# Optimization experiments

Measured on AMD Instinct MI355X. Metric: run time of the kernel, lower is better.

## Reference

```python
import jax, jax.numpy as jnp
import numpy as np

B, D, H, W_ = 2, 256, 64, 64


def setup_inputs() -> dict:
    key = jax.random.key(0)
    k1, k2 = jax.random.split(key)
    x = jax.random.normal(k1, (B, D, H, W_), dtype=jnp.float32)
    W = jax.random.normal(k2, (3 * D, D), dtype=jnp.float32) * 0.02  # 1x1 conv weight [out,in]
    b = jnp.zeros((3 * D,), dtype=jnp.float32)
    return {"x": x, "W": W, "b": b}


def reference(x, W, b):
    Bs, d, h, w = x.shape
    N = h * w
    sqrtV = d ** 0.25  # sqrt(sqrt(d)); q,k each divided -> qk^T / sqrt(d)
    # 1x1 conv == per-pixel linear over channels
    qkv = jnp.einsum('bchw,oc->bohw', x, W) + b[None, :, None, None]
    q, k, v = jnp.split(qkv, 3, axis=1)
    q = q.reshape(Bs, d, N).transpose(0, 2, 1) / sqrtV  # [B,N,d]
    k = k.reshape(Bs, d, N).transpose(0, 2, 1) / sqrtV
    v = v.reshape(Bs, d, N).transpose(0, 2, 1)
    # Sinkhorn (eps=1, max_iter=1, uniform marginals 1/N), log domain.
    # cost C = -q k^T  =>  -C = q k^T (softmax-style logits)
    negC = jnp.einsum('bnd,bmd->bnm', q, k)  # [B,N,N]
    logm = jnp.log(1.0 / N + 1e-8).astype(x.dtype)
    u = logm - jax.nn.logsumexp(negC, axis=-1)            # [B,N] row update
    vpot = logm - jax.nn.logsumexp(negC + u[..., None], axis=-2)  # [B,N] col update
    pi = jnp.exp(negC + u[..., None] + vpot[:, None, :])  # transport plan = attn
    out = jnp.einsum('bnm,bmd->bnd', pi, v)               # [B,N,d]
    return out.transpose(0, 2, 1).reshape(Bs, d, h, w)
```

## Files before the change

kernel.cpp:

```cpp
#include <hip/hip_runtime.h>
#include <hip/hip_bf16.h>
#include <math.h>

typedef __bf16 bf16;
typedef __bf16 bf16x8 __attribute__((ext_vector_type(8)));
typedef __bf16 bf16x4 __attribute__((ext_vector_type(4)));
typedef float floatx4 __attribute__((ext_vector_type(4)));

typedef const __attribute__((address_space(1))) void* gas_t;
typedef __attribute__((address_space(3))) void* las_t;

#define NPIX 4096
#define DCH 256

#define OFF_XB   ((size_t)0)
#define OFF_WB   ((size_t)4194304)
#define OFF_Q    ((size_t)4587520)
#define OFF_K    ((size_t)8781824)
#define OFF_V    ((size_t)12976128)
#define OFF_E    ((size_t)17170432)
#define OFF_VPP  ((size_t)84279296)
#define OFF_RP   ((size_t)88473600)
#define OFF_CP   ((size_t)89522176)
#define OFF_PART ((size_t)90570752)

__device__ __forceinline__ void stage_tile(const bf16* __restrict__ g0, size_t rstride,
                                           bf16* lds, int t) {
  const int wbase = (t >> 6) << 6;
#pragma unroll
  for (int i = 0; i < 4; i++) {
    int slot = i * 256 + t;
    int row = slot >> 3, seg = slot & 7;
    const bf16* g = g0 + (size_t)row * rstride + ((seg ^ (row & 7)) << 3);
    bf16* l = lds + (size_t)(i * 256 + wbase) * 8;
    __builtin_amdgcn_global_load_lds((gas_t)g, (las_t)l, 16, 0, 0);
  }
}

__global__ __launch_bounds__(256) void prep(
    const float* __restrict__ x, const float* __restrict__ W,
    bf16* __restrict__ xb, bf16* __restrict__ wb)
{
  const int t = threadIdx.x;
  if (blockIdx.y == 4) {
    int gid = (blockIdx.z * 64 + blockIdx.x) * 256 + t;
    for (int i = gid; i < 49152; i += 32768) {
      float4 v = *(const float4*)(W + (size_t)i * 4);
      bf16x4 pk = { (bf16)v.x, (bf16)v.y, (bf16)v.z, (bf16)v.w };
      *(bf16x4*)(wb + (size_t)i * 4) = pk;
    }
    return;
  }
  __shared__ float ts[64][65];
  const int b = blockIdx.z, n0 = blockIdx.x * 64, c0 = blockIdx.y * 64;
  const float* xp = x + ((size_t)b * DCH + c0) * NPIX + n0;
  for (int i = 0; i < 4; i++) {
    int slot = t + i * 256;
    int c = slot >> 4, nq = (slot & 15) * 4;
    float4 v = *(const float4*)(xp + (size_t)c * NPIX + nq);
    ts[c][nq + 0] = v.x; ts[c][nq + 1] = v.y; ts[c][nq + 2] = v.z; ts[c][nq + 3] = v.w;
  }
  __syncthreads();
  for (int i = 0; i < 2; i++) {
    int slot = t + i * 256;
    int n = slot >> 3, cq = (slot & 7) * 8;
    bf16x8 pk;
    for (int j = 0; j < 8; j++) pk[j] = (bf16)ts[cq + j][n];
    *(bf16x8*)(xb + ((size_t)b * NPIX + n0 + n) * DCH + c0 + cq) = pk;
  }
}

__global__ __launch_bounds__(256) void conv_mfma(
    const bf16* __restrict__ xb, const bf16* __restrict__ wb,
    const float* __restrict__ bias,
    bf16* __restrict__ qb, bf16* __restrict__ kb, bf16* __restrict__ vb)
{
  __shared__ bf16 at[128 * 64];
  __shared__ bf16 bt[128 * 64];
  __shared__ float bs[128];
  const int t  = threadIdx.x;
  const int n0 = blockIdx.x * 128;
  const int o0 = blockIdx.y * 128;
  if (t < 128) bs[t] = bias[o0 + t];
  const int lane = t & 63, wave = t >> 6;
  const int wm = wave >> 1, wn = wave & 1;
  const int l15 = lane & 15, quad = lane >> 4;
  const int l7 = l15 & 7;

  floatx4 acc[4][4];
  for (int i=0;i<4;i++) for (int j=0;j<4;j++) for (int r=0;r<4;r++) acc[i][j][r] = 0.f;

  for (int k0 = 0; k0 < DCH; k0 += 64) {
    stage_tile(wb + (size_t)o0 * DCH + k0, DCH, at, t);
    stage_tile(xb + (size_t)n0 * DCH + k0, DCH, bt, t);
    __syncthreads();
    for (int kk = 0; kk < 2; kk++) {
      bf16x8 af[4], bfr[4];
      int sw = ((kk * 4 + quad) ^ l7) * 8;
      for (int f = 0; f < 4; f++)
        af[f]  = *(const bf16x8*)&at[(wm*64 + f*16 + l15)*64 + sw];
      for (int f = 0; f < 4; f++)
        bfr[f] = *(const bf16x8*)&bt[(wn*64 + f*16 + l15)*64 + sw];
      for (int fm = 0; fm < 4; fm++)
        for (int fn = 0; fn < 4; fn++)
          acc[fm][fn] = __builtin_amdgcn_mfma_f32_16x16x32_bf16(af[fm], bfr[fn], acc[fm][fn], 0, 0, 0);
    }
    __syncthreads();
  }

  const float scale = (o0 < 512) ? 0.25f : 1.0f;
  bf16* dst; int od;
  if (o0 < 256)      { dst = qb; od = o0; }
  else if (o0 < 512) { dst = kb; od = o0 - 256; }
  else               { dst = vb; od = o0 - 512; }

  for (int fm = 0; fm < 4; fm++)
    for (int fn = 0; fn < 4; fn++) {
      int o_l = wm*64 + fm*16 + quad*4;
      int n_g = n0 + wn*64 + fn*16 + l15;
      bf16x4 pk;
      for (int r = 0; r < 4; r++)
        pk[r] = (bf16)((acc[fm][fn][r] + bs[o_l + r]) * scale);
      *(bf16x4*)(dst + (size_t)n_g * DCH + od + o_l) = pk;
    }
}

__global__ __launch_bounds__(256) void pass_a(
    const bf16* __restrict__ qb, const bf16* __restrict__ kb,
    bf16* __restrict__ E, float* __restrict__ rowpartG)
{
  __shared__ bf16 kt[128 * 64];
  __shared__ bf16 qt[128 * 64];
  __shared__ float rowpart[128];
  const int b = blockIdx.z;
  qb += (size_t)b * NPIX * DCH;
  kb += (size_t)b * NPIX * DCH;
  E  += (size_t)b * NPIX * NPIX;
  float* rp = rowpartG + ((size_t)b * 32 + blockIdx.x) * NPIX;
  const int t  = threadIdx.x;
  const int m0 = blockIdx.x * 128;
  const int n0 = blockIdx.y * 128;
  const int lane = t & 63, wave = t >> 6;
  const int wm = wave >> 1, wn = wave & 1;
  const int l15 = lane & 15, quad = lane >> 4;
  const int l7 = l15 & 7;

  floatx4 acc[4][4];
  for (int i=0;i<4;i++) for (int j=0;j<4;j++) for (int r=0;r<4;r++) acc[i][j][r] = 0.f;

  for (int k0 = 0; k0 < DCH; k0 += 64) {
    stage_tile(kb + (size_t)m0 * DCH + k0, DCH, kt, t);
    stage_tile(qb + (size_t)n0 * DCH + k0, DCH, qt, t);
    __syncthreads();
    for (int kk = 0; kk < 2; kk++) {
      bf16x8 af[4], bfr[4];
      int sw = ((kk * 4 + quad) ^ l7) * 8;
      for (int f = 0; f < 4; f++)
        af[f]  = *(const bf16x8*)&kt[(wm*64 + f*16 + l15)*64 + sw];
      for (int f = 0; f < 4; f++)
        bfr[f] = *(const bf16x8*)&qt[(wn*64 + f*16 + l15)*64 + sw];
      for (int fm = 0; fm < 4; fm++)
        for (int fn = 0; fn < 4; fn++)
          acc[fm][fn] = __builtin_amdgcn_mfma_f32_16x16x32_bf16(af[fm], bfr[fn], acc[fm][fn], 0, 0, 0);
    }
    __syncthreads();
  }

  if (t < 128) rowpart[t] = 0.f;
  __syncthreads();

  float rsum[4] = {0.f, 0.f, 0.f, 0.f};
  for (int fm = 0; fm < 4; fm++)
    for (int fn = 0; fn < 4; fn++) {
      int n_g = n0 + wn*64 + fn*16 + l15;
      int m_g = m0 + wm*64 + fm*16 + quad*4;
      bf16x4 pk;
      float s = 0.f;
      for (int r = 0; r < 4; r++) {
        float e = __expf(acc[fm][fn][r]);
        pk[r] = (bf16)e;
        s += e;
      }
      *(bf16x4*)(E + (size_t)n_g * NPIX + m_g) = pk;
      rsum[fn] += s;
    }
  for (int fn = 0; fn < 4; fn++) {
    float s = rsum[fn];
    s += __shfl_xor(s, 16);
    s += __shfl_xor(s, 32);
    if (quad == 0) atomicAdd(&rowpart[wn*64 + fn*16 + l15], s);
  }
  __syncthreads();
  if (t < 128) rp[n0 + t] = rowpart[t];
}

__global__ __launch_bounds__(256) void col_pass(
    const bf16* __restrict__ E, const float* __restrict__ rowpartG,
    float* __restrict__ colpartG, float logm)
{
  __shared__ float eus[128];
  const int b = blockIdx.z;
  E += (size_t)b * NPIX * NPIX;
  const float* rp = rowpartG + (size_t)b * 32 * NPIX;
  float* cp = colpartG + ((size_t)b * 32 + blockIdx.y) * NPIX;
  const int t = threadIdx.x;
  const int col = blockIdx.x * 1024 + t * 4;
  const int nbase = blockIdx.y * 128;
  if (t < 128) {
    float s = 0.f;
    for (int mi = 0; mi < 32; mi++) s += rp[(size_t)mi * NPIX + nbase + t];
    eus[t] = __expf(logm - __logf(s));
  }
  __syncthreads();
  float a0 = 0.f, a1 = 0.f, a2 = 0.f, a3 = 0.f;
  for (int r = 0; r < 128; r++) {
    float eu = eus[r];
    bf16x4 ev = *(const bf16x4*)(E + (size_t)(nbase + r) * NPIX + col);
    a0 += eu * (float)ev[0];
    a1 += eu * (float)ev[1];
    a2 += eu * (float)ev[2];
    a3 += eu * (float)ev[3];
  }
  float4 o = {a0, a1, a2, a3};
  *(float4*)(cp + col) = o;
}

__global__ __launch_bounds__(256) void vpp_kernel(
    const bf16* __restrict__ vb, const float* __restrict__ colpartG,
    bf16* __restrict__ vppT, float logm)
{
  __shared__ float ts[64][65];
  __shared__ float ef[64];
  const int b = blockIdx.z;
  vb += (size_t)b * NPIX * DCH;
  const float* cp = colpartG + (size_t)b * 32 * NPIX;
  vppT += (size_t)b * DCH * NPIX;
  const int t = threadIdx.x;
  const int m0 = blockIdx.x * 64, d0 = blockIdx.y * 64;
  if (t < 64) {
    float s = 0.f;
    for (int g = 0; g < 32; g++) s += cp[(size_t)g * NPIX + m0 + t];
    ef[t] = __expf(logm - __logf(s));
  }
  __syncthreads();
  for (int i = 0; i < 2; i++) {
    int slot = t + i * 256;
    int m = slot >> 3, dq = (slot & 7) * 8;
    bf16x8 v = *(const bf16x8*)(vb + (size_t)(m0 + m) * DCH + d0 + dq);
    float s = ef[m];
    for (int j = 0; j < 8; j++) ts[dq + j][m] = s * (float)v[j];
  }
  __syncthreads();
  for (int i = 0; i < 2; i++) {
    int slot = t + i * 256;
    int d = slot >> 3, mq = (slot & 7) * 8;
    bf16x8 pk;
    for (int j = 0; j < 8; j++) pk[j] = (bf16)ts[d][mq + j];
    *(bf16x8*)(vppT + (size_t)(d0 + d) * NPIX + m0 + mq) = pk;
  }
}

__global__ __launch_bounds__(256) void pass_c(
    const bf16* __restrict__ E, const bf16* __restrict__ vppT,
    const float* __restrict__ rowpartG, bf16* __restrict__ part, float logm)
{
  __shared__ bf16 et[128 * 64];
  __shared__ bf16 vt[128 * 64];
  __shared__ float eus[128];
  const int z = blockIdx.z;
  const int b = z >> 2, kc = z & 3;
  E += (size_t)b * NPIX * NPIX;
  vppT += (size_t)b * DCH * NPIX;
  const float* rp = rowpartG + (size_t)b * 32 * NPIX;
  part += (size_t)(b * 4 + kc) * DCH * NPIX;
  const int t  = threadIdx.x;
  const int n0 = blockIdx.x * 128;
  const int d0 = blockIdx.y * 128;
  const int mstart = kc * 1024;
  if (t < 128) {
    float s = 0.f;
    for (int mi = 0; mi < 32; mi++) s += rp[(size_t)mi * NPIX + n0 + t];
    eus[t] = __expf(logm - __logf(s));
  }
  const int lane = t & 63, wave = t >> 6;
  const int wn = wave >> 1, wd = wave & 1;
  const int l15 = lane & 15, quad = lane >> 4;
  const int l7 = l15 & 7;

  floatx4 acc[4][4];
  for (int i=0;i<4;i++) for (int j=0;j<4;j++) for (int r=0;r<4;r++) acc[i][j][r] = 0.f;
  __syncthreads();

  for (int k0 = mstart; k0 < mstart + 1024; k0 += 64) {
    stage_tile(E + (size_t)n0 * NPIX + k0, NPIX, et, t);
    stage_tile(vppT + (size_t)d0 * NPIX + k0, NPIX, vt, t);
    __syncthreads();
    for (int kk = 0; kk < 2; kk++) {
      bf16x8 af[4], bfr[4];
      int sw = ((kk * 4 + quad) ^ l7) * 8;
      for (int f = 0; f < 4; f++)
        af[f]  = *(const bf16x8*)&et[(wn*64 + f*16 + l15)*64 + sw];
      for (int f = 0; f < 4; f++)
        bfr[f] = *(const bf16x8*)&vt[(wd*64 + f*16 + l15)*64 + sw];
      for (int fn = 0; fn < 4; fn++)
        for (int fd = 0; fd < 4; fd++)
          acc[fn][fd] = __builtin_amdgcn_mfma_f32_16x16x32_bf16(af[fn], bfr[fd], acc[fn][fd], 0, 0, 0);
    }
    __syncthreads();
  }

  for (int fn = 0; fn < 4; fn++)
    for (int fd = 0; fd < 4; fd++) {
      int d_g = d0 + wd*64 + fd*16 + l15;
      int n_l = wn*64 + fn*16 + quad*4;
      bf16x4 o;
      o[0] = (bf16)(acc[fn][fd][0] * eus[n_l + 0]);
      o[1] = (bf16)(acc[fn][fd][1] * eus[n_l + 1]);
      o[2] = (bf16)(acc[fn][fd][2] * eus[n_l + 2]);
      o[3] = (bf16)(acc[fn][fd][3] * eus[n_l + 3]);
      *(bf16x4*)(part + (size_t)d_g * NPIX + n0 + n_l) = o;
    }
}

__global__ __launch_bounds__(256) void reduce_k(
    const bf16* __restrict__ part, float* __restrict__ outp)
{
  size_t i4 = ((size_t)blockIdx.x * 256 + threadIdx.x) * 4;
  size_t b = i4 >> 20;
  size_t off = i4 & (size_t)1048575;
  const bf16* p = part + b * 4 * (size_t)1048576 + off;
  bf16x4 a = *(const bf16x4*)(p);
  bf16x4 bq = *(const bf16x4*)(p + (size_t)1048576);
  bf16x4 c = *(const bf16x4*)(p + (size_t)2097152);
  bf16x4 d = *(const bf16x4*)(p + (size_t)3145728);
  float4 s = { (float)a[0]+(float)bq[0]+(float)c[0]+(float)d[0],
               (float)a[1]+(float)bq[1]+(float)c[1]+(float)d[1],
               (float)a[2]+(float)bq[2]+(float)c[2]+(float)d[2],
               (float)a[3]+(float)bq[3]+(float)c[3]+(float)d[3] };
  *(float4*)(outp + i4) = s;
}

extern "C" void kernel_launch(void* const* d_in, const int* in_sizes, int n_in,
                              void* d_out, int out_size, void* d_ws, size_t ws_size,
                              hipStream_t stream) {
  (void)in_sizes; (void)n_in; (void)out_size; (void)ws_size;
  const float* x    = (const float*)d_in[0];
  const float* Wm   = (const float*)d_in[1];
  const float* bias = (const float*)d_in[2];
  float* outp = (float*)d_out;
  char* ws = (char*)d_ws;

  bf16*  xb   = (bf16*)(ws + OFF_XB);
  bf16*  wb   = (bf16*)(ws + OFF_WB);
  bf16*  qb   = (bf16*)(ws + OFF_Q);
  bf16*  kb   = (bf16*)(ws + OFF_K);
  bf16*  vb   = (bf16*)(ws + OFF_V);
  bf16*  E    = (bf16*)(ws + OFF_E);
  bf16*  vppT = (bf16*)(ws + OFF_VPP);
  float* rp   = (float*)(ws + OFF_RP);
  float* cp   = (float*)(ws + OFF_CP);
  bf16*  part = (bf16*)(ws + OFF_PART);

  const float logm = logf(1.0f / 4096.0f + 1e-8f);

  prep<<<dim3(64, 5, 2), 256, 0, stream>>>(x, Wm, xb, wb);
  conv_mfma<<<dim3(64, 6), 256, 0, stream>>>(xb, wb, bias, qb, kb, vb);

  pass_a<<<dim3(32, 32, 2), 256, 0, stream>>>(qb, kb, E, rp);
  col_pass<<<dim3(4, 32, 2), 256, 0, stream>>>(E, rp, cp, logm);
  vpp_kernel<<<dim3(64, 4, 2), 256, 0, stream>>>(vb, cp, vppT, logm);
  pass_c<<<dim3(32, 2, 8), 256, 0, stream>>>(E, vppT, rp, part, logm);
  reduce_k<<<2048, 256, 0, stream>>>(part, outp);
}
```

Measured before the change: 160.1 us.

## Fuse fp32-to-bf16 prep into conv GEMM and widen col_pass loads

Removes the separate prep kernel: conv_mfma now reads fp32 x and W directly, converts them to bf16 and stores into padded LDS tiles (stride 72) instead of using async global_load_lds from pre-converted buffers. This saves one launch and the round trip of writing and re-reading xb/wb. In exchange, the conv kernel does strided scalar fp32 loads of x and conversions in its inner loop. col_pass is also reshaped to 64-row groups with 8-wide bf16 loads, which doubles the column partials that vpp_kernel must sum.

After: 161.4 us. Within noise of the previous version (+0.8%).

```diff
diff --git a/kernel.cpp b/kernel.cpp
--- a/kernel.cpp
+++ b/kernel.cpp
@@ -12,17 +12,17 @@
 
 #define NPIX 4096
 #define DCH 256
-
-#define OFF_XB   ((size_t)0)
-#define OFF_WB   ((size_t)4194304)
-#define OFF_Q    ((size_t)4587520)
-#define OFF_K    ((size_t)8781824)
-#define OFF_V    ((size_t)12976128)
-#define OFF_E    ((size_t)17170432)
-#define OFF_VPP  ((size_t)84279296)
-#define OFF_RP   ((size_t)88473600)
-#define OFF_CP   ((size_t)89522176)
-#define OFF_PART ((size_t)90570752)
+#define LSTR 72
+
+#define MB ((size_t)1048576)
+#define OFF_Q    ((size_t)0)
+#define OFF_K    (4*MB)
+#define OFF_V    (8*MB)
+#define OFF_E    (12*MB)
+#define OFF_VPP  (76*MB)
+#define OFF_RP   (80*MB)
+#define OFF_CP   (81*MB)
+#define OFF_PART (83*MB)
 
 __device__ __forceinline__ void stage_tile(const bf16* __restrict__ g0, size_t rstride,
                                            bf16* lds, int t) {
@@ -37,70 +37,51 @@
   }
 }
 
-__global__ __launch_bounds__(256) void prep(
+__global__ __launch_bounds__(256) void conv_mfma(
     const float* __restrict__ x, const float* __restrict__ W,
-    bf16* __restrict__ xb, bf16* __restrict__ wb)
-{
-  const int t = threadIdx.x;
-  if (blockIdx.y == 4) {
-    int gid = (blockIdx.z * 64 + blockIdx.x) * 256 + t;
-    for (int i = gid; i < 49152; i += 32768) {
-      float4 v = *(const float4*)(W + (size_t)i * 4);
-      bf16x4 pk = { (bf16)v.x, (bf16)v.y, (bf16)v.z, (bf16)v.w };
-      *(bf16x4*)(wb + (size_t)i * 4) = pk;
-    }
-    return;
-  }
-  __shared__ float ts[64][65];
-  const int b = blockIdx.z, n0 = blockIdx.x * 64, c0 = blockIdx.y * 64;
-  const float* xp = x + ((size_t)b * DCH + c0) * NPIX + n0;
-  for (int i = 0; i < 4; i++) {
-    int slot = t + i * 256;
-    int c = slot >> 4, nq = (slot & 15) * 4;
-    float4 v = *(const float4*)(xp + (size_t)c * NPIX + nq);
-    ts[c][nq + 0] = v.x; ts[c][nq + 1] = v.y; ts[c][nq + 2] = v.z; ts[c][nq + 3] = v.w;
-  }
-  __syncthreads();
-  for (int i = 0; i < 2; i++) {
-    int slot = t + i * 256;
-    int n = slot >> 3, cq = (slot & 7) * 8;
-    bf16x8 pk;
-    for (int j = 0; j < 8; j++) pk[j] = (bf16)ts[cq + j][n];
-    *(bf16x8*)(xb + ((size_t)b * NPIX + n0 + n) * DCH + c0 + cq) = pk;
-  }
-}
-
-__global__ __launch_bounds__(256) void conv_mfma(
-    const bf16* __restrict__ xb, const bf16* __restrict__ wb,
     const float* __restrict__ bias,
     bf16* __restrict__ qb, bf16* __restrict__ kb, bf16* __restrict__ vb)
 {
-  __shared__ bf16 at[128 * 64];
-  __shared__ bf16 bt[128 * 64];
+  __shared__ bf16 at[128 * LSTR];
+  __shared__ bf16 bt[128 * LSTR];
   __shared__ float bs[128];
   const int t  = threadIdx.x;
+  const int bz = blockIdx.z;
   const int n0 = blockIdx.x * 128;
   const int o0 = blockIdx.y * 128;
   if (t < 128) bs[t] = bias[o0 + t];
+  const float* xp = x + (size_t)bz * DCH * NPIX;
   const int lane = t & 63, wave = t >> 6;
   const int wm = wave >> 1, wn = wave & 1;
   const int l15 = lane & 15, quad = lane >> 4;
-  const int l7 = l15 & 7;
 
   floatx4 acc[4][4];
   for (int i=0;i<4;i++) for (int j=0;j<4;j++) for (int r=0;r<4;r++) acc[i][j][r] = 0.f;
 
   for (int k0 = 0; k0 < DCH; k0 += 64) {
-    stage_tile(wb + (size_t)o0 * DCH + k0, DCH, at, t);
-    stage_tile(xb + (size_t)n0 * DCH + k0, DCH, bt, t);
+#pragma unroll
+    for (int i = 0; i < 8; i++) {
+      int slot = i * 256 + t;
+      int row = slot >> 4, cq = (slot & 15) * 4;
+      float4 v = *(const float4*)(W + (size_t)(o0 + row) * DCH + k0 + cq);
+      bf16x4 pk = { (bf16)v.x, (bf16)v.y, (bf16)v.z, (bf16)v.w };
+      *(bf16x4*)&at[row * LSTR + cq] = pk;
+    }
+#pragma unroll
+    for (int i = 0; i < 8; i++) {
+      int slot = i * 256 + t;
+      int nl = slot & 127, cq = (slot >> 7) * 4;
+      const float* xs = xp + (size_t)(k0 + cq) * NPIX + n0 + nl;
+      bf16x4 pk = { (bf16)xs[0], (bf16)xs[NPIX], (bf16)xs[2 * NPIX], (bf16)xs[3 * NPIX] };
+      *(bf16x4*)&bt[nl * LSTR + cq] = pk;
+    }
     __syncthreads();
     for (int kk = 0; kk < 2; kk++) {
       bf16x8 af[4], bfr[4];
-      int sw = ((kk * 4 + quad) ^ l7) * 8;
-      for (int f = 0; f < 4; f++)
-        af[f]  = *(const bf16x8*)&at[(wm*64 + f*16 + l15)*64 + sw];
-      for (int f = 0; f < 4; f++)
-        bfr[f] = *(const bf16x8*)&bt[(wn*64 + f*16 + l15)*64 + sw];
+      for (int f = 0; f < 4; f++)
+        af[f]  = *(const bf16x8*)&at[(wm*64 + f*16 + l15)*LSTR + kk*32 + quad*8];
+      for (int f = 0; f < 4; f++)
+        bfr[f] = *(const bf16x8*)&bt[(wn*64 + f*16 + l15)*LSTR + kk*32 + quad*8];
       for (int fm = 0; fm < 4; fm++)
         for (int fn = 0; fn < 4; fn++)
           acc[fm][fn] = __builtin_amdgcn_mfma_f32_16x16x32_bf16(af[fm], bfr[fn], acc[fm][fn], 0, 0, 0);
@@ -113,6 +94,7 @@
   if (o0 < 256)      { dst = qb; od = o0; }
   else if (o0 < 512) { dst = kb; od = o0 - 256; }
   else               { dst = vb; od = o0 - 512; }
+  dst += (size_t)bz * NPIX * DCH;
 
   for (int fm = 0; fm < 4; fm++)
     for (int fn = 0; fn < 4; fn++) {
@@ -198,31 +180,31 @@
     const bf16* __restrict__ E, const float* __restrict__ rowpartG,
     float* __restrict__ colpartG, float logm)
 {
-  __shared__ float eus[128];
+  __shared__ float eus[64];
   const int b = blockIdx.z;
   E += (size_t)b * NPIX * NPIX;
   const float* rp = rowpartG + (size_t)b * 32 * NPIX;
-  float* cp = colpartG + ((size_t)b * 32 + blockIdx.y) * NPIX;
+  float* cp = colpartG + ((size_t)b * 64 + blockIdx.y) * NPIX;
   const int t = threadIdx.x;
-  const int col = blockIdx.x * 1024 + t * 4;
-  const int nbase = blockIdx.y * 128;
-  if (t < 128) {
+  const int col = blockIdx.x * 2048 + t * 8;
+  const int nbase = blockIdx.y * 64;
+  if (t < 64) {
     float s = 0.f;
     for (int mi = 0; mi < 32; mi++) s += rp[(size_t)mi * NPIX + nbase + t];
     eus[t] = __expf(logm - __logf(s));
   }
   __syncthreads();
-  float a0 = 0.f, a1 = 0.f, a2 = 0.f, a3 = 0.f;
-  for (int r = 0; r < 128; r++) {
+  float a[8];
+  for (int i = 0; i < 8; i++) a[i] = 0.f;
+  for (int r = 0; r < 64; r++) {
     float eu = eus[r];
-    bf16x4 ev = *(const bf16x4*)(E + (size_t)(nbase + r) * NPIX + col);
-    a0 += eu * (float)ev[0];
-    a1 += eu * (float)ev[1];
-    a2 += eu * (float)ev[2];
-    a3 += eu * (float)ev[3];
-  }
-  float4 o = {a0, a1, a2, a3};
-  *(float4*)(cp + col) = o;
+    bf16x8 ev = *(const bf16x8*)(E + (size_t)(nbase + r) * NPIX + col);
+    for (int i = 0; i < 8; i++) a[i] += eu * (float)ev[i];
+  }
+  float4 o0 = {a[0], a[1], a[2], a[3]};
+  float4 o1 = {a[4], a[5], a[6], a[7]};
+  *(float4*)(cp + col) = o0;
+  *(float4*)(cp + col + 4) = o1;
 }
 
 __global__ __launch_bounds__(256) void vpp_kernel(
@@ -233,13 +215,13 @@
   __shared__ float ef[64];
   const int b = blockIdx.z;
   vb += (size_t)b * NPIX * DCH;
-  const float* cp = colpartG + (size_t)b * 32 * NPIX;
+  const float* cp = colpartG + (size_t)b * 64 * NPIX;
   vppT += (size_t)b * DCH * NPIX;
   const int t = threadIdx.x;
   const int m0 = blockIdx.x * 64, d0 = blockIdx.y * 64;
   if (t < 64) {
     float s = 0.f;
-    for (int g = 0; g < 32; g++) s += cp[(size_t)g * NPIX + m0 + t];
+    for (int g = 0; g < 64; g++) s += cp[(size_t)g * NPIX + m0 + t];
     ef[t] = __expf(logm - __logf(s));
   }
   __syncthreads();
@@ -350,8 +332,6 @@
   float* outp = (float*)d_out;
   char* ws = (char*)d_ws;
 
-  bf16*  xb   = (bf16*)(ws + OFF_XB);
-  bf16*  wb   = (bf16*)(ws + OFF_WB);
   bf16*  qb   = (bf16*)(ws + OFF_Q);
   bf16*  kb   = (bf16*)(ws + OFF_K);
   bf16*  vb   = (bf16*)(ws + OFF_V);
@@ -363,11 +343,9 @@
 
   const float logm = logf(1.0f / 4096.0f + 1e-8f);
 
-  prep<<<dim3(64, 5, 2), 256, 0, stream>>>(x, Wm, xb, wb);
-  conv_mfma<<<dim3(64, 6), 256, 0, stream>>>(xb, wb, bias, qb, kb, vb);
-
+  conv_mfma<<<dim3(32, 6, 2), 256, 0, stream>>>(x, Wm, bias, qb, kb, vb);
   pass_a<<<dim3(32, 32, 2), 256, 0, stream>>>(qb, kb, E, rp);
-  col_pass<<<dim3(4, 32, 2), 256, 0, stream>>>(E, rp, cp, logm);
+  col_pass<<<dim3(2, 64, 2), 256, 0, stream>>>(E, rp, cp, logm);
   vpp_kernel<<<dim3(64, 4, 2), 256, 0, stream>>>(vb, cp, vppT, logm);
   pass_c<<<dim3(32, 2, 8), 256, 0, stream>>>(E, vppT, rp, part, logm);
   reduce_k<<<2048, 256, 0, stream>>>(part, outp);
```
